# Kernel tuning notes

Measured on AMD Instinct MI355X. Metric: run time of the kernel, lower is better.

## Reference

```python
import jax, jax.numpy as jnp
import numpy as np
from jax.ops import segment_sum

N_NODES = 100000


def setup_inputs() -> dict:
    key = jax.random.key(0)
    k1, k2, k3, k4, k5 = jax.random.split(key, 5)
    E = 3200000
    x = jax.random.normal(k1, (N_NODES, 8), dtype=jnp.float32)
    edge_index = jax.random.randint(k2, (2, E), 0, N_NODES, dtype=jnp.int64)
    edge_attr = jax.random.uniform(k3, (E,), dtype=jnp.float32)
    W = jax.random.normal(k4, (8, 64), dtype=jnp.float32) * (1.0 / np.sqrt(8.0))
    b = jax.random.normal(k5, (64,), dtype=jnp.float32) * 0.01
    return {"x": x, "edge_index": edge_index, "edge_attr": edge_attr, "W": W, "b": b}


def reference(x, edge_index, edge_attr, W, b):
    # GCNConv(8, 64) with symmetric normalization and self-loops (PyG defaults).
    N = x.shape[0]
    # Add self-loops with weight 1.0
    loops = jnp.arange(N, dtype=edge_index.dtype)
    row = jnp.concatenate([edge_index[0], loops])            # source nodes [E+N]
    col = jnp.concatenate([edge_index[1], loops])            # target nodes [E+N]
    ew = jnp.concatenate([edge_attr, jnp.ones((N,), dtype=edge_attr.dtype)])
    # Symmetric degree normalization: deg computed on target index
    deg = segment_sum(ew, col, num_segments=N)               # [N]
    dis = jnp.where(deg > 0, jax.lax.rsqrt(jnp.where(deg > 0, deg, 1.0)), 0.0)
    norm = dis[row] * ew * dis[col]                          # [E+N]
    # Linear transform first (in=8 -> out=64), then gather/scale/scatter-add
    xt = x @ W                                               # [N, 64]
    msgs = xt[row] * norm[:, None]                           # [E+N, 64]
    out = segment_sum(msgs, col, num_segments=N) + b         # [N, 64]
    return out
```

## Files before the change

### kernel.cpp

```cpp
#include <hip/hip_runtime.h>


#define NBMAX 1024
#define PSH   7
#define BINSZ 128
#define TILE  6144
#define EPT   6
#define CAP   6144

static inline size_t ws_align(size_t x) { return (x + 255) & ~(size_t)255; }

__global__ void init_k(const unsigned* w, unsigned* orw, unsigned* cnt, int E) {
    int t = threadIdx.x;
    for (int i = t; i < NBMAX; i += 256) cnt[i] = 0u;
    __shared__ unsigned s;
    if (t == 0) s = 0u;
    __syncthreads();
    unsigned v = 0;
    int lim = (E < 2048) ? E : 2048;
    for (int i = t; i < lim; i += 256)
        v |= w[2 * i + 1];
    atomicOr(&s, v);
    __syncthreads();
    if (t == 0) *orw = s;
}

__global__ void hist_k(const void* ei, const unsigned* orw, unsigned* cnt,
                       int E, int NB) {
    __shared__ unsigned lh[NBMAX];
    const bool is64 = (*orw == 0u);
    const int* e32 = (const int*)ei;
    const long long* e64 = (const long long*)ei;
    for (int i = threadIdx.x; i < NB; i += blockDim.x) lh[i] = 0u;
    __syncthreads();
    int t = blockIdx.x * blockDim.x + threadIdx.x;
    int st = gridDim.x * blockDim.x;
    for (int e = t; e < E; e += st) {
        int c = is64 ? (int)e64[E + e] : e32[E + e];
        atomicAdd(&lh[c >> PSH], 1u);
    }
    __syncthreads();
    for (int i = threadIdx.x; i < NB; i += blockDim.x) {
        unsigned v = lh[i];
        if (v) atomicAdd(&cnt[i], v);
    }
}

__global__ void scan_k(const unsigned* cnt, unsigned* offs, unsigned* gcur, int NB) {
    __shared__ unsigned wsum[16];
    int t = threadIdx.x, lane = t & 63, wv = t >> 6;
    unsigned v0 = (t < NB) ? cnt[t] : 0u;
    unsigned s = v0;
    #pragma unroll
    for (int d = 1; d < 64; d <<= 1) {
        unsigned u = __shfl_up(s, d);
        if (lane >= d) s += u;
    }
    if (lane == 63) wsum[wv] = s;
    __syncthreads();
    if (t < 16) {
        unsigned w = wsum[t];
        #pragma unroll
        for (int d = 1; d < 16; d <<= 1) {
            unsigned u = __shfl_up(w, d, 16);
            if (t >= d) w += u;
        }
        wsum[t] = w;
    }
    __syncthreads();
    unsigned excl = s - v0 + (wv ? wsum[wv - 1] : 0u);
    if (t < NB) { offs[t] = excl; gcur[t] = excl; }
    if (t == NB - 1) offs[NB] = excl + v0;
}

__global__ __launch_bounds__(1024)
void scat_k(const void* ei, const float* ea, const unsigned* orw,
            unsigned* gcur, unsigned long long* pay, int E, int NB, int ntiles) {
    __shared__ unsigned long long lp[TILE];
    __shared__ unsigned short lbin[TILE];
    __shared__ unsigned lh[NBMAX];
    __shared__ unsigned lo[NBMAX];
    __shared__ unsigned gb[NBMAX];
    __shared__ unsigned wsum[16];
    const bool is64 = (*orw == 0u);
    const int* e32 = (const int*)ei;
    const long long* e64 = (const long long*)ei;
    const int t = threadIdx.x, lane = t & 63, wv = t >> 6;

    for (int tile = blockIdx.x; tile < ntiles; tile += gridDim.x) {
        int base = tile * TILE;
        int tc = E - base; if (tc > TILE) tc = TILE;

        for (int i = t; i < NB; i += 1024) lh[i] = 0u;
        __syncthreads();

        int bn[EPT]; unsigned rk[EPT]; unsigned long long pv[EPT];
        #pragma unroll
        for (int i = 0; i < EPT; ++i) {
            int e = base + i * 1024 + t;
            bn[i] = -1;
            if (e < base + tc) {
                int c, r;
                if (is64) { c = (int)e64[E + e]; r = (int)e64[e]; }
                else      { c = e32[E + e];      r = e32[e]; }
                float w = ea[e];
                bn[i] = c >> PSH;
                pv[i] = ((unsigned long long)__float_as_uint(w) << 32)
                        | ((unsigned)r << 8) | (unsigned)(c & (BINSZ - 1));
                rk[i] = atomicAdd(&lh[bn[i]], 1u);
            }
        }
        __syncthreads();

        unsigned v0 = (t < NB) ? lh[t] : 0u;
        unsigned s = v0;
        #pragma unroll
        for (int d = 1; d < 64; d <<= 1) {
            unsigned u = __shfl_up(s, d);
            if (lane >= d) s += u;
        }
        if (lane == 63) wsum[wv] = s;
        __syncthreads();
        if (t < 16) {
            unsigned w = wsum[t];
            #pragma unroll
            for (int d = 1; d < 16; d <<= 1) {
                unsigned u = __shfl_up(w, d, 16);
                if (t >= d) w += u;
            }
            wsum[t] = w;
        }
        __syncthreads();
        unsigned excl = s - v0 + (wv ? wsum[wv - 1] : 0u);
        if (t < NB) {
            lo[t] = excl;
            if (v0) gb[t] = atomicAdd(&gcur[t], v0);
        }
        __syncthreads();

        #pragma unroll
        for (int i = 0; i < EPT; ++i)
            if (bn[i] >= 0) {
                unsigned pos = lo[bn[i]] + rk[i];
                lp[pos] = pv[i];
                lbin[pos] = (unsigned short)bn[i];
            }
        __syncthreads();

        for (int q = t; q < tc; q += 1024) {
            int a = lbin[q];
            pay[(size_t)gb[a] + (unsigned)q - lo[a]] = lp[q];
        }
        __syncthreads();
    }
}

__global__ __launch_bounds__(1024)
void nodestat_k(const unsigned long long* pay, const unsigned* offs,
                unsigned* noffs, float* dis, const float* x, float* y,
                int N, int E) {
    __shared__ unsigned cnt[BINSZ];
    __shared__ float dw[BINSZ];
    __shared__ float sdis[BINSZ];
    __shared__ unsigned wpart[2];
    int b = blockIdx.x, t = threadIdx.x, lane = t & 63, wv = t >> 6;
    if (t < BINSZ) { cnt[t] = 0u; dw[t] = 0.f; }
    if (b == 0 && t == 0) noffs[N] = (unsigned)E;
    __syncthreads();
    unsigned base = offs[b], len = offs[b + 1] - base;
    for (unsigned j = t; j < len; j += 1024) {
        unsigned long long p = pay[base + j];
        unsigned lc = (unsigned)p & 255u;
        atomicAdd(&cnt[lc], 1u);
        atomicAdd(&dw[lc], __uint_as_float((unsigned)(p >> 32)));
    }
    __syncthreads();
    unsigned v0 = (t < BINSZ) ? cnt[t] : 0u;
    unsigned s = v0;
    #pragma unroll
    for (int d = 1; d < 64; d <<= 1) {
        unsigned u = __shfl_up(s, d);
        if (lane >= d) s += u;
    }
    if (t < BINSZ && lane == 63) wpart[wv] = s;
    __syncthreads();
    if (t < BINSZ) {
        unsigned excl = s - v0 + (wv == 1 ? wpart[0] : 0u);
        int node = b * BINSZ + t;
        float dval = 0.f;
        if (node < N) {
            noffs[node] = base + excl;
            float d = 1.0f + dw[t];
            dval = (d > 0.f) ? rsqrtf(d) : 0.f;
            dis[node] = dval;
        }
        sdis[t] = dval;
    }
    __syncthreads();
    int gi = b * (BINSZ * 8) + t;
    if (gi < N * 8) y[gi] = sdis[t >> 3] * x[gi];
}

__global__ __launch_bounds__(1024)
void aggfuse_k(const unsigned long long* pay, const unsigned* offs,
               const unsigned* noffs, const float* dis, const float* y,
               const float* Wm, const float* bv, float* out, int N) {
    __shared__ unsigned long long lp[CAP];
    __shared__ float spill[BINSZ][8];
    __shared__ float sag[BINSZ][8];
    __shared__ unsigned loc[BINSZ];
    __shared__ unsigned cur[BINSZ];
    const float4* y4 = (const float4*)y;
    int b = blockIdx.x, t = threadIdx.x, lane = t & 63, wv = t >> 6;
    unsigned base = offs[b], len = offs[b + 1] - base;
    ((float*)spill)[t] = 0.f;
    if (t < BINSZ) {
        int node = b * BINSZ + t;
        unsigned l = (node < N) ? (noffs[node] - base) : len;
        loc[t] = l; cur[t] = l;
    }
    __syncthreads();
    for (unsigned j = t; j < len; j += 1024) {
        unsigned long long p = pay[base + j];
        unsigned lc = (unsigned)p & 255u;
        unsigned pos = atomicAdd(&cur[lc], 1u);
        if (pos < CAP) lp[pos] = p;
        else {
            unsigned r = ((unsigned)p >> 8) & 0xFFFFFFu;
            float ew = __uint_as_float((unsigned)(p >> 32));
            float4 u = y4[(size_t)r * 2], v = y4[(size_t)r * 2 + 1];
            atomicAdd(&spill[lc][0], ew * u.x); atomicAdd(&spill[lc][1], ew * u.y);
            atomicAdd(&spill[lc][2], ew * u.z); atomicAdd(&spill[lc][3], ew * u.w);
            atomicAdd(&spill[lc][4], ew * v.x); atomicAdd(&spill[lc][5], ew * v.y);
            atomicAdd(&spill[lc][6], ew * v.z); atomicAdd(&spill[lc][7], ew * v.w);
        }
    }
    __syncthreads();
    int half = lane >> 5;
    int l5 = lane & 31;
    int slot = l5 >> 1, h = l5 & 1;
    for (int i = 0; i < 4; ++i) {
        int ln = wv + ((2 * i + half) << 4);
        int node = b * BINSZ + ln;
        float a0 = 0.f, a1 = 0.f, a2 = 0.f, a3 = 0.f;
        if (node < N) {
            unsigned s = loc[ln] + slot;
            unsigned e = (ln < BINSZ - 1) ? loc[ln + 1] : len;
            e = e < CAP ? e : CAP;
            for (unsigned j = s; j < e; j += 16) {
                unsigned long long p = lp[j];
                unsigned r = ((unsigned)p >> 8) & 0xFFFFFFu;
                float ew = __uint_as_float((unsigned)(p >> 32));
                float4 v = y4[(size_t)r * 2 + h];
                a0 += ew * v.x; a1 += ew * v.y; a2 += ew * v.z; a3 += ew * v.w;
            }
        }
        #pragma unroll
        for (int m = 2; m <= 16; m <<= 1) {
            a0 += __shfl_xor(a0, m); a1 += __shfl_xor(a1, m);
            a2 += __shfl_xor(a2, m); a3 += __shfl_xor(a3, m);
        }
        if (slot == 0 && node < N) {
            float dc = dis[node];
            float4 vy = y4[(size_t)node * 2 + h];
            sag[ln][h * 4 + 0] = dc * (a0 + spill[ln][h * 4 + 0] + vy.x);
            sag[ln][h * 4 + 1] = dc * (a1 + spill[ln][h * 4 + 1] + vy.y);
            sag[ln][h * 4 + 2] = dc * (a2 + spill[ln][h * 4 + 2] + vy.z);
            sag[ln][h * 4 + 3] = dc * (a3 + spill[ln][h * 4 + 3] + vy.w);
        }
    }
    __syncthreads();
    float wr[8];
    #pragma unroll
    for (int k = 0; k < 8; ++k) wr[k] = Wm[k * 64 + lane];
    float bj = bv[lane];
    for (int i = 0; i < 8; ++i) {
        int ln = wv + (i << 4);
        int node = b * BINSZ + ln;
        if (node < N) {
            float o = bj;
            #pragma unroll
            for (int k = 0; k < 8; ++k) o += sag[ln][k] * wr[k];
            out[(size_t)node * 64 + lane] = o;
        }
    }
}

__global__ void fb_init_k(float* deg, float4* agg4, int N) {
    int i = blockIdx.x * blockDim.x + threadIdx.x, st = gridDim.x * blockDim.x;
    for (; i < N; i += st) {
        deg[i] = 1.0f;
        agg4[2 * i] = make_float4(0.f, 0.f, 0.f, 0.f);
        agg4[2 * i + 1] = make_float4(0.f, 0.f, 0.f, 0.f);
    }
}
__global__ void fb_deg_k(const void* ei, const float* ea, const unsigned* orw,
                         float* deg, int E) {
    const bool is64 = (*orw == 0u);
    const int* e32 = (const int*)ei;
    const long long* e64 = (const long long*)ei;
    int e = blockIdx.x * blockDim.x + threadIdx.x, st = gridDim.x * blockDim.x;
    for (; e < E; e += st) {
        int c = is64 ? (int)e64[E + e] : e32[E + e];
        atomicAdd(&deg[c], ea[e]);
    }
}
__global__ void fb_dis_k(float* deg, int N) {
    int i = blockIdx.x * blockDim.x + threadIdx.x, st = gridDim.x * blockDim.x;
    for (; i < N; i += st) {
        float d = deg[i];
        deg[i] = (d > 0.f) ? rsqrtf(d) : 0.f;
    }
}
__global__ void fb_edge_k(const void* ei, const float* ea, const unsigned* orw,
                          const float* dis, const float* x, float* agg, int E) {
    const bool is64 = (*orw == 0u);
    const int* e32 = (const int*)ei;
    const long long* e64 = (const long long*)ei;
    int e = blockIdx.x * blockDim.x + threadIdx.x, st = gridDim.x * blockDim.x;
    for (; e < E; e += st) {
        int r, c;
        if (is64) { r = (int)e64[e]; c = (int)e64[E + e]; }
        else      { r = e32[e];      c = e32[E + e]; }
        float nrm = dis[r] * ea[e] * dis[c];
        const float4* xr = (const float4*)(x + (size_t)r * 8);
        float4 a = xr[0], bb = xr[1];
        float* ag = agg + (size_t)c * 8;
        atomicAdd(ag + 0, nrm * a.x);  atomicAdd(ag + 1, nrm * a.y);
        atomicAdd(ag + 2, nrm * a.z);  atomicAdd(ag + 3, nrm * a.w);
        atomicAdd(ag + 4, nrm * bb.x); atomicAdd(ag + 5, nrm * bb.y);
        atomicAdd(ag + 6, nrm * bb.z); atomicAdd(ag + 7, nrm * bb.w);
    }
}
__global__ void fb_out_k(const float* x, const float* Wm, const float* bv,
                         const float* dis, const float* agg, float* out, int N) {
    int lane = threadIdx.x & 63;
    int wid = blockIdx.x * (blockDim.x >> 6) + (threadIdx.x >> 6);
    int nw = gridDim.x * (blockDim.x >> 6);
    float wr[8];
    #pragma unroll
    for (int k = 0; k < 8; ++k) wr[k] = Wm[k * 64 + lane];
    float bj = bv[lane];
    for (int i = wid; i < N; i += nw) {
        float d = dis[i];
        float ink = 0.f;
        if (lane < 8) ink = agg[(size_t)i * 8 + lane] + d * d * x[(size_t)i * 8 + lane];
        float acc = bj;
        #pragma unroll
        for (int k = 0; k < 8; ++k) acc += __shfl(ink, k) * wr[k];
        out[(size_t)i * 64 + lane] = acc;
    }
}

extern "C" void kernel_launch(void* const* d_in, const int* in_sizes, int n_in,
                              void* d_out, int out_size, void* d_ws, size_t ws_size,
                              hipStream_t stream) {
    const float* x  = (const float*)d_in[0];
    const void*  ei = d_in[1];
    const float* ea = (const float*)d_in[2];
    const float* Wm = (const float*)d_in[3];
    const float* bv = (const float*)d_in[4];
    float* out = (float*)d_out;

    const int N = in_sizes[0] / 8;
    const int E = in_sizes[2];
    const int NB = (N + BINSZ - 1) / BINSZ;

    char* ws = (char*)d_ws;
    size_t o = 0;
    unsigned* orw   = (unsigned*)(ws + o); o += 256;
    unsigned* cnt   = (unsigned*)(ws + o); o += ws_align(NBMAX * 4);
    unsigned* offs  = (unsigned*)(ws + o); o += ws_align((NBMAX + 1) * 4);
    unsigned* gcur  = (unsigned*)(ws + o); o += ws_align(NBMAX * 4);
    float* dis      = (float*)(ws + o);    o += ws_align((size_t)N * 4);
    unsigned* noffs = (unsigned*)(ws + o); o += ws_align((size_t)(N + 1) * 4);
    float* y        = (float*)(ws + o);    o += ws_align((size_t)N * 8 * 4);
    unsigned long long* pay = (unsigned long long*)(ws + o);
    o += ws_align((size_t)E * 8);

    const int ntiles = (E + TILE - 1) / TILE;

    if (NB <= NBMAX && E >= 2048 && o <= ws_size) {
        init_k<<<1, 256, 0, stream>>>((const unsigned*)ei, orw, cnt, E);
        hist_k<<<256, 512, 0, stream>>>(ei, orw, cnt, E, NB);
        scan_k<<<1, 1024, 0, stream>>>(cnt, offs, gcur, NB);
        scat_k<<<ntiles, 1024, 0, stream>>>(ei, ea, orw, gcur, pay, E, NB, ntiles);
        nodestat_k<<<NB, 1024, 0, stream>>>(pay, offs, noffs, dis, x, y, N, E);
        aggfuse_k<<<NB, 1024, 0, stream>>>(pay, offs, noffs, dis, y, Wm, bv, out, N);
    } else {
        float* agg = (float*)(ws + 256 + ws_align((size_t)N * 4));
        init_k<<<1, 256, 0, stream>>>((const unsigned*)ei, orw, cnt, E);
        fb_init_k<<<(N + 255) / 256, 256, 0, stream>>>(dis, (float4*)agg, N);
        fb_deg_k<<<2048, 256, 0, stream>>>(ei, ea, orw, dis, E);
        fb_dis_k<<<(N + 255) / 256, 256, 0, stream>>>(dis, N);
        fb_edge_k<<<2048, 256, 0, stream>>>(ei, ea, orw, dis, x, agg, E);
        fb_out_k<<<2048, 256, 0, stream>>>(x, Wm, bv, dis, agg, out, N);
    }
}
```

Baseline: 114.5 us.

## Replace atomic bin cursors with per-tile histogram and column scan

The binning sort now computes a histogram per tile and runs a column-wise exclusive scan over tiles (scan2_k). This gives every tile a fixed global base per bin, so the scatter kernel no longer needs global atomics on the bin cursors. It also drops the shared-memory staging and local scan, writing payloads directly from the shared rank atomics. In exchange it adds an extra pass over column indices, a per-tile count array of ntiles*NB entries, and another launch, and the direct writes are less coalesced.

```diff
diff --git a/kernel.cpp b/kernel.cpp
--- a/kernel.cpp
+++ b/kernel.cpp
@@ -5,14 +5,12 @@
 #define PSH   7
 #define BINSZ 128
 #define TILE  6144
-#define EPT   6
 #define CAP   6144
 
 static inline size_t ws_align(size_t x) { return (x + 255) & ~(size_t)255; }
 
-__global__ void init_k(const unsigned* w, unsigned* orw, unsigned* cnt, int E) {
+__global__ void init_k(const unsigned* w, unsigned* orw, int E) {
     int t = threadIdx.x;
-    for (int i = t; i < NBMAX; i += 256) cnt[i] = 0u;
     __shared__ unsigned s;
     if (t == 0) s = 0u;
     __syncthreads();
@@ -25,28 +23,49 @@
     if (t == 0) *orw = s;
 }
 
-__global__ void hist_k(const void* ei, const unsigned* orw, unsigned* cnt,
-                       int E, int NB) {
+__global__ __launch_bounds__(1024)
+void hist_k(const void* ei, const unsigned* orw, unsigned* tcnt,
+            int E, int NB, int ntiles) {
     __shared__ unsigned lh[NBMAX];
     const bool is64 = (*orw == 0u);
     const int* e32 = (const int*)ei;
     const long long* e64 = (const long long*)ei;
-    for (int i = threadIdx.x; i < NB; i += blockDim.x) lh[i] = 0u;
-    __syncthreads();
-    int t = blockIdx.x * blockDim.x + threadIdx.x;
-    int st = gridDim.x * blockDim.x;
-    for (int e = t; e < E; e += st) {
-        int c = is64 ? (int)e64[E + e] : e32[E + e];
-        atomicAdd(&lh[c >> PSH], 1u);
-    }
-    __syncthreads();
-    for (int i = threadIdx.x; i < NB; i += blockDim.x) {
-        unsigned v = lh[i];
-        if (v) atomicAdd(&cnt[i], v);
-    }
-}
-
-__global__ void scan_k(const unsigned* cnt, unsigned* offs, unsigned* gcur, int NB) {
+    const int t = threadIdx.x;
+    for (int tile = blockIdx.x; tile < ntiles; tile += gridDim.x) {
+        int base = tile * TILE;
+        int tc = E - base; if (tc > TILE) tc = TILE;
+        for (int i = t; i < NB; i += 1024) lh[i] = 0u;
+        __syncthreads();
+        for (int e = base + t; e < base + tc; e += 1024) {
+            int c = is64 ? (int)e64[E + e] : e32[E + e];
+            atomicAdd(&lh[c >> PSH], 1u);
+        }
+        __syncthreads();
+        for (int i = t; i < NB; i += 1024)
+            tcnt[(size_t)tile * NB + i] = lh[i];
+        __syncthreads();
+    }
+}
+
+__global__ void scan2_k(unsigned* tcnt, unsigned* cnt, int NB, int ntiles) {
+    int b = blockIdx.x, lane = threadIdx.x;
+    unsigned run = 0;
+    for (int base = 0; base < ntiles; base += 64) {
+        int i = base + lane;
+        unsigned v = (i < ntiles) ? tcnt[(size_t)i * NB + b] : 0u;
+        unsigned s = v;
+        #pragma unroll
+        for (int d = 1; d < 64; d <<= 1) {
+            unsigned u = __shfl_up(s, d);
+            if (lane >= d) s += u;
+        }
+        if (i < ntiles) tcnt[(size_t)i * NB + b] = run + s - v;
+        run += __shfl(s, 63);
+    }
+    if (lane == 0) cnt[b] = run;
+}
+
+__global__ void scan_k(const unsigned* cnt, unsigned* offs, int NB) {
     __shared__ unsigned wsum[16];
     int t = threadIdx.x, lane = t & 63, wv = t >> 6;
     unsigned v0 = (t < NB) ? cnt[t] : 0u;
@@ -69,87 +88,38 @@
     }
     __syncthreads();
     unsigned excl = s - v0 + (wv ? wsum[wv - 1] : 0u);
-    if (t < NB) { offs[t] = excl; gcur[t] = excl; }
+    if (t < NB) offs[t] = excl;
     if (t == NB - 1) offs[NB] = excl + v0;
 }
 
 __global__ __launch_bounds__(1024)
 void scat_k(const void* ei, const float* ea, const unsigned* orw,
-            unsigned* gcur, unsigned long long* pay, int E, int NB, int ntiles) {
-    __shared__ unsigned long long lp[TILE];
-    __shared__ unsigned short lbin[TILE];
+            const unsigned* offs, const unsigned* tcnt,
+            unsigned long long* pay, int E, int NB, int ntiles) {
+    __shared__ unsigned tb[NBMAX];
     __shared__ unsigned lh[NBMAX];
-    __shared__ unsigned lo[NBMAX];
-    __shared__ unsigned gb[NBMAX];
-    __shared__ unsigned wsum[16];
     const bool is64 = (*orw == 0u);
     const int* e32 = (const int*)ei;
     const long long* e64 = (const long long*)ei;
-    const int t = threadIdx.x, lane = t & 63, wv = t >> 6;
-
+    const int t = threadIdx.x;
     for (int tile = blockIdx.x; tile < ntiles; tile += gridDim.x) {
         int base = tile * TILE;
         int tc = E - base; if (tc > TILE) tc = TILE;
-
-        for (int i = t; i < NB; i += 1024) lh[i] = 0u;
-        __syncthreads();
-
-        int bn[EPT]; unsigned rk[EPT]; unsigned long long pv[EPT];
-        #pragma unroll
-        for (int i = 0; i < EPT; ++i) {
-            int e = base + i * 1024 + t;
-            bn[i] = -1;
-            if (e < base + tc) {
-                int c, r;
-                if (is64) { c = (int)e64[E + e]; r = (int)e64[e]; }
-                else      { c = e32[E + e];      r = e32[e]; }
-                float w = ea[e];
-                bn[i] = c >> PSH;
-                pv[i] = ((unsigned long long)__float_as_uint(w) << 32)
-                        | ((unsigned)r << 8) | (unsigned)(c & (BINSZ - 1));
-                rk[i] = atomicAdd(&lh[bn[i]], 1u);
-            }
-        }
-        __syncthreads();
-
-        unsigned v0 = (t < NB) ? lh[t] : 0u;
-        unsigned s = v0;
-        #pragma unroll
-        for (int d = 1; d < 64; d <<= 1) {
-            unsigned u = __shfl_up(s, d);
-            if (lane >= d) s += u;
-        }
-        if (lane == 63) wsum[wv] = s;
-        __syncthreads();
-        if (t < 16) {
-            unsigned w = wsum[t];
-            #pragma unroll
-            for (int d = 1; d < 16; d <<= 1) {
-                unsigned u = __shfl_up(w, d, 16);
-                if (t >= d) w += u;
-            }
-            wsum[t] = w;
-        }
-        __syncthreads();
-        unsigned excl = s - v0 + (wv ? wsum[wv - 1] : 0u);
-        if (t < NB) {
-            lo[t] = excl;
-            if (v0) gb[t] = atomicAdd(&gcur[t], v0);
-        }
-        __syncthreads();
-
-        #pragma unroll
-        for (int i = 0; i < EPT; ++i)
-            if (bn[i] >= 0) {
-                unsigned pos = lo[bn[i]] + rk[i];
-                lp[pos] = pv[i];
-                lbin[pos] = (unsigned short)bn[i];
-            }
-        __syncthreads();
-
-        for (int q = t; q < tc; q += 1024) {
-            int a = lbin[q];
-            pay[(size_t)gb[a] + (unsigned)q - lo[a]] = lp[q];
+        for (int i = t; i < NB; i += 1024) {
+            tb[i] = offs[i] + tcnt[(size_t)tile * NB + i];
+            lh[i] = 0u;
+        }
+        __syncthreads();
+        for (int e = base + t; e < base + tc; e += 1024) {
+            int c, r;
+            if (is64) { c = (int)e64[E + e]; r = (int)e64[e]; }
+            else      { c = e32[E + e];      r = e32[e]; }
+            float w = ea[e];
+            int bn = c >> PSH;
+            unsigned rk = atomicAdd(&lh[bn], 1u);
+            pay[(size_t)tb[bn] + rk] =
+                ((unsigned long long)__float_as_uint(w) << 32)
+                | ((unsigned)r << 8) | (unsigned)(c & (BINSZ - 1));
         }
         __syncthreads();
     }
@@ -365,31 +335,32 @@
     const int N = in_sizes[0] / 8;
     const int E = in_sizes[2];
     const int NB = (N + BINSZ - 1) / BINSZ;
+    const int ntiles = (E + TILE - 1) / TILE;
 
     char* ws = (char*)d_ws;
     size_t o = 0;
     unsigned* orw   = (unsigned*)(ws + o); o += 256;
     unsigned* cnt   = (unsigned*)(ws + o); o += ws_align(NBMAX * 4);
     unsigned* offs  = (unsigned*)(ws + o); o += ws_align((NBMAX + 1) * 4);
-    unsigned* gcur  = (unsigned*)(ws + o); o += ws_align(NBMAX * 4);
     float* dis      = (float*)(ws + o);    o += ws_align((size_t)N * 4);
     unsigned* noffs = (unsigned*)(ws + o); o += ws_align((size_t)(N + 1) * 4);
     float* y        = (float*)(ws + o);    o += ws_align((size_t)N * 8 * 4);
+    unsigned* tcnt  = (unsigned*)(ws + o); o += ws_align((size_t)ntiles * NB * 4);
     unsigned long long* pay = (unsigned long long*)(ws + o);
     o += ws_align((size_t)E * 8);
 
-    const int ntiles = (E + TILE - 1) / TILE;
-
     if (NB <= NBMAX && E >= 2048 && o <= ws_size) {
-        init_k<<<1, 256, 0, stream>>>((const unsigned*)ei, orw, cnt, E);
-        hist_k<<<256, 512, 0, stream>>>(ei, orw, cnt, E, NB);
-        scan_k<<<1, 1024, 0, stream>>>(cnt, offs, gcur, NB);
-        scat_k<<<ntiles, 1024, 0, stream>>>(ei, ea, orw, gcur, pay, E, NB, ntiles);
+        int hgrid = ntiles < 2048 ? ntiles : 2048;
+        init_k<<<1, 256, 0, stream>>>((const unsigned*)ei, orw, E);
+        hist_k<<<hgrid, 1024, 0, stream>>>(ei, orw, tcnt, E, NB, ntiles);
+        scan2_k<<<NB, 64, 0, stream>>>(tcnt, cnt, NB, ntiles);
+        scan_k<<<1, 1024, 0, stream>>>(cnt, offs, NB);
+        scat_k<<<hgrid, 1024, 0, stream>>>(ei, ea, orw, offs, tcnt, pay, E, NB, ntiles);
         nodestat_k<<<NB, 1024, 0, stream>>>(pay, offs, noffs, dis, x, y, N, E);
         aggfuse_k<<<NB, 1024, 0, stream>>>(pay, offs, noffs, dis, y, Wm, bv, out, N);
     } else {
         float* agg = (float*)(ws + 256 + ws_align((size_t)N * 4));
-        init_k<<<1, 256, 0, stream>>>((const unsigned*)ei, orw, cnt, E);
+        init_k<<<1, 256, 0, stream>>>((const unsigned*)ei, orw, E);
         fb_init_k<<<(N + 255) / 256, 256, 0, stream>>>(dis, (float4*)agg, N);
         fb_deg_k<<<2048, 256, 0, stream>>>(ei, ea, orw, dis, E);
         fb_dis_k<<<(N + 255) / 256, 256, 0, stream>>>(dis, N);
```

New measurement: 127.9 us. 1.12x slower.

## Replace atomic bin cursors with per-tile histograms and deterministic scatter offsets

Applied to the files above, without the earlier changes.

The histogram pass now writes a per-tile count for each bin, and a new column-wise scan kernel turns those counts into per-tile exclusive offsets. The scatter kernel then computes its global write positions directly instead of reserving them with atomics on a shared cursor array, and it walks tiles in an interleaved order. The aggregation loop in the later kernel is also remapped from 16 to 8 lanes per node so each wave handles four nodes at a time. This removes global atomic contention and makes the edge ordering deterministic, at the cost of an extra kernel launch and a per-tile count buffer that is written and read back.

```diff
diff --git a/kernel.cpp b/kernel.cpp
--- a/kernel.cpp
+++ b/kernel.cpp
@@ -10,9 +10,8 @@
 
 static inline size_t ws_align(size_t x) { return (x + 255) & ~(size_t)255; }
 
-__global__ void init_k(const unsigned* w, unsigned* orw, unsigned* cnt, int E) {
+__global__ void init_k(const unsigned* w, unsigned* orw, int E) {
     int t = threadIdx.x;
-    for (int i = t; i < NBMAX; i += 256) cnt[i] = 0u;
     __shared__ unsigned s;
     if (t == 0) s = 0u;
     __syncthreads();
@@ -25,28 +24,49 @@
     if (t == 0) *orw = s;
 }
 
-__global__ void hist_k(const void* ei, const unsigned* orw, unsigned* cnt,
-                       int E, int NB) {
+__global__ __launch_bounds__(1024)
+void hist_k(const void* ei, const unsigned* orw, unsigned* tcnt,
+            int E, int NB, int ntiles) {
     __shared__ unsigned lh[NBMAX];
     const bool is64 = (*orw == 0u);
     const int* e32 = (const int*)ei;
     const long long* e64 = (const long long*)ei;
-    for (int i = threadIdx.x; i < NB; i += blockDim.x) lh[i] = 0u;
-    __syncthreads();
-    int t = blockIdx.x * blockDim.x + threadIdx.x;
-    int st = gridDim.x * blockDim.x;
-    for (int e = t; e < E; e += st) {
-        int c = is64 ? (int)e64[E + e] : e32[E + e];
-        atomicAdd(&lh[c >> PSH], 1u);
-    }
-    __syncthreads();
-    for (int i = threadIdx.x; i < NB; i += blockDim.x) {
-        unsigned v = lh[i];
-        if (v) atomicAdd(&cnt[i], v);
-    }
-}
-
-__global__ void scan_k(const unsigned* cnt, unsigned* offs, unsigned* gcur, int NB) {
+    const int t = threadIdx.x;
+    for (int tile = blockIdx.x; tile < ntiles; tile += gridDim.x) {
+        int base = tile * TILE;
+        int tc = E - base; if (tc > TILE) tc = TILE;
+        for (int i = t; i < NB; i += 1024) lh[i] = 0u;
+        __syncthreads();
+        for (int e = base + t; e < base + tc; e += 1024) {
+            int c = is64 ? (int)e64[E + e] : e32[E + e];
+            atomicAdd(&lh[c >> PSH], 1u);
+        }
+        __syncthreads();
+        for (int i = t; i < NB; i += 1024)
+            tcnt[(size_t)tile * NB + i] = lh[i];
+        __syncthreads();
+    }
+}
+
+__global__ void scan2_k(unsigned* tcnt, unsigned* cnt, int NB, int ntiles) {
+    int b = blockIdx.x, lane = threadIdx.x;
+    unsigned run = 0;
+    for (int base = 0; base < ntiles; base += 64) {
+        int i = base + lane;
+        unsigned v = (i < ntiles) ? tcnt[(size_t)i * NB + b] : 0u;
+        unsigned s = v;
+        #pragma unroll
+        for (int d = 1; d < 64; d <<= 1) {
+            unsigned u = __shfl_up(s, d);
+            if (lane >= d) s += u;
+        }
+        if (i < ntiles) tcnt[(size_t)i * NB + b] = run + s - v;
+        run += __shfl(s, 63);
+    }
+    if (lane == 0) cnt[b] = run;
+}
+
+__global__ void scan_k(const unsigned* cnt, unsigned* offs, int NB) {
     __shared__ unsigned wsum[16];
     int t = threadIdx.x, lane = t & 63, wv = t >> 6;
     unsigned v0 = (t < NB) ? cnt[t] : 0u;
@@ -69,25 +89,29 @@
     }
     __syncthreads();
     unsigned excl = s - v0 + (wv ? wsum[wv - 1] : 0u);
-    if (t < NB) { offs[t] = excl; gcur[t] = excl; }
+    if (t < NB) offs[t] = excl;
     if (t == NB - 1) offs[NB] = excl + v0;
 }
 
 __global__ __launch_bounds__(1024)
 void scat_k(const void* ei, const float* ea, const unsigned* orw,
-            unsigned* gcur, unsigned long long* pay, int E, int NB, int ntiles) {
+            const unsigned* offs, const unsigned* tcnt,
+            unsigned long long* pay, int E, int NB, int ntiles, int cpx) {
     __shared__ unsigned long long lp[TILE];
     __shared__ unsigned short lbin[TILE];
     __shared__ unsigned lh[NBMAX];
     __shared__ unsigned lo[NBMAX];
-    __shared__ unsigned gb[NBMAX];
+    __shared__ unsigned tb[NBMAX];
     __shared__ unsigned wsum[16];
     const bool is64 = (*orw == 0u);
     const int* e32 = (const int*)ei;
     const long long* e64 = (const long long*)ei;
     const int t = threadIdx.x, lane = t & 63, wv = t >> 6;
-
-    for (int tile = blockIdx.x; tile < ntiles; tile += gridDim.x) {
+    const int sgrid = cpx * 8;
+
+    for (int ii = blockIdx.x; ii < sgrid; ii += gridDim.x) {
+        int tile = (ii & 7) * cpx + (ii >> 3);
+        if (tile >= ntiles) continue;
         int base = tile * TILE;
         int tc = E - base; if (tc > TILE) tc = TILE;
 
@@ -134,7 +158,7 @@
         unsigned excl = s - v0 + (wv ? wsum[wv - 1] : 0u);
         if (t < NB) {
             lo[t] = excl;
-            if (v0) gb[t] = atomicAdd(&gcur[t], v0);
+            tb[t] = offs[t] + tcnt[(size_t)tile * NB + t];
         }
         __syncthreads();
 
@@ -149,7 +173,7 @@
 
         for (int q = t; q < tc; q += 1024) {
             int a = lbin[q];
-            pay[(size_t)gb[a] + (unsigned)q - lo[a]] = lp[q];
+            pay[(size_t)tb[a] + (unsigned)q - lo[a]] = lp[q];
         }
         __syncthreads();
     }
@@ -236,18 +260,18 @@
         }
     }
     __syncthreads();
-    int half = lane >> 5;
-    int l5 = lane & 31;
-    int slot = l5 >> 1, h = l5 & 1;
-    for (int i = 0; i < 4; ++i) {
-        int ln = wv + ((2 * i + half) << 4);
+    int quad = lane >> 4;
+    int l4 = lane & 15;
+    int slot = l4 >> 1, h = l4 & 1;
+    for (int i = 0; i < 2; ++i) {
+        int ln = wv + ((4 * i + quad) << 4);
         int node = b * BINSZ + ln;
         float a0 = 0.f, a1 = 0.f, a2 = 0.f, a3 = 0.f;
         if (node < N) {
             unsigned s = loc[ln] + slot;
             unsigned e = (ln < BINSZ - 1) ? loc[ln + 1] : len;
             e = e < CAP ? e : CAP;
-            for (unsigned j = s; j < e; j += 16) {
+            for (unsigned j = s; j < e; j += 8) {
                 unsigned long long p = lp[j];
                 unsigned r = ((unsigned)p >> 8) & 0xFFFFFFu;
                 float ew = __uint_as_float((unsigned)(p >> 32));
@@ -256,7 +280,7 @@
             }
         }
         #pragma unroll
-        for (int m = 2; m <= 16; m <<= 1) {
+        for (int m = 2; m <= 8; m <<= 1) {
             a0 += __shfl_xor(a0, m); a1 += __shfl_xor(a1, m);
             a2 += __shfl_xor(a2, m); a3 += __shfl_xor(a3, m);
         }
@@ -365,31 +389,35 @@
     const int N = in_sizes[0] / 8;
     const int E = in_sizes[2];
     const int NB = (N + BINSZ - 1) / BINSZ;
+    const int ntiles = (E + TILE - 1) / TILE;
+    const int cpx = (ntiles + 7) / 8;
 
     char* ws = (char*)d_ws;
     size_t o = 0;
     unsigned* orw   = (unsigned*)(ws + o); o += 256;
     unsigned* cnt   = (unsigned*)(ws + o); o += ws_align(NBMAX * 4);
     unsigned* offs  = (unsigned*)(ws + o); o += ws_align((NBMAX + 1) * 4);
-    unsigned* gcur  = (unsigned*)(ws + o); o += ws_align(NBMAX * 4);
     float* dis      = (float*)(ws + o);    o += ws_align((size_t)N * 4);
     unsigned* noffs = (unsigned*)(ws + o); o += ws_align((size_t)(N + 1) * 4);
     float* y        = (float*)(ws + o);    o += ws_align((size_t)N * 8 * 4);
+    unsigned* tcnt  = (unsigned*)(ws + o); o += ws_align((size_t)ntiles * NB * 4);
     unsigned long long* pay = (unsigned long long*)(ws + o);
     o += ws_align((size_t)E * 8);
 
-    const int ntiles = (E + TILE - 1) / TILE;
-
     if (NB <= NBMAX && E >= 2048 && o <= ws_size) {
-        init_k<<<1, 256, 0, stream>>>((const unsigned*)ei, orw, cnt, E);
-        hist_k<<<256, 512, 0, stream>>>(ei, orw, cnt, E, NB);
-        scan_k<<<1, 1024, 0, stream>>>(cnt, offs, gcur, NB);
-        scat_k<<<ntiles, 1024, 0, stream>>>(ei, ea, orw, gcur, pay, E, NB, ntiles);
+        int hgrid = ntiles < 2048 ? ntiles : 2048;
+        int sgrid = cpx * 8 < 2048 ? cpx * 8 : 2048;
+        init_k<<<1, 256, 0, stream>>>((const unsigned*)ei, orw, E);
+        hist_k<<<hgrid, 1024, 0, stream>>>(ei, orw, tcnt, E, NB, ntiles);
+        scan2_k<<<NB, 64, 0, stream>>>(tcnt, cnt, NB, ntiles);
+        scan_k<<<1, 1024, 0, stream>>>(cnt, offs, NB);
+        scat_k<<<sgrid, 1024, 0, stream>>>(ei, ea, orw, offs, tcnt, pay, E, NB,
+                                           ntiles, cpx);
         nodestat_k<<<NB, 1024, 0, stream>>>(pay, offs, noffs, dis, x, y, N, E);
         aggfuse_k<<<NB, 1024, 0, stream>>>(pay, offs, noffs, dis, y, Wm, bv, out, N);
     } else {
         float* agg = (float*)(ws + 256 + ws_align((size_t)N * 4));
-        init_k<<<1, 256, 0, stream>>>((const unsigned*)ei, orw, cnt, E);
+        init_k<<<1, 256, 0, stream>>>((const unsigned*)ei, orw, E);
         fb_init_k<<<(N + 255) / 256, 256, 0, stream>>>(dis, (float4*)agg, N);
         fb_deg_k<<<2048, 256, 0, stream>>>(ei, ea, orw, dis, E);
         fb_dis_k<<<(N + 255) / 256, 256, 0, stream>>>(dis, N);
```

Measured after the change: 108.2 us. 1.06x faster.
